# Kernel tuning notes

Hardware: AMD Instinct MI355X
Metric: run time of the kernel (lower is better)

The kernel has to match this reference:

```python
import math
import jax, jax.numpy as jnp
import numpy as np

B, T, C = 4, 2048, 2048
LAYER_ID, N_LAYER = 12, 24


def setup_inputs() -> dict:
    key = jax.random.key(0)
    kx, kk, kv, kr, ko = jax.random.split(key, 5)
    x = jax.random.normal(kx, (B, T, C), dtype=jnp.float32)

    # parameter init faithful to the torch __init__
    ratio_1_to_almost0 = 1.0 - LAYER_ID / N_LAYER
    ratio_0_to_1 = LAYER_ID / (N_LAYER - 1)
    h = np.arange(C, dtype=np.float64)
    zigzag = (((np.arange(C) + 1) % 3) - 1) * 0.5
    time_first = jnp.asarray(np.ones(C) * math.log(0.3) + zigzag, dtype=jnp.float32)
    base = (h / C)  # x[0,0,i] = i / n_embed
    time_mix_k = jnp.asarray((base ** ratio_1_to_almost0)[None, None, :], dtype=jnp.float32)
    time_mix_v = jnp.asarray((base ** ratio_1_to_almost0 + 0.3 * ratio_0_to_1)[None, None, :], dtype=jnp.float32)
    time_mix_r = jnp.asarray((base ** (0.5 * ratio_1_to_almost0))[None, None, :], dtype=jnp.float32)
    xx = jnp.ones((1, 1, C), dtype=jnp.float32)
    aa = jnp.ones((1, 1, C), dtype=jnp.float32)
    bb = jnp.ones((1, 1, C), dtype=jnp.float32)
    pp = jnp.full((1, 1, C), -1e30, dtype=jnp.float32)

    scale = 0.02
    w_key = jax.random.normal(kk, (C, C), dtype=jnp.float32) * scale
    w_value = jax.random.normal(kv, (C, C), dtype=jnp.float32) * scale
    w_rec = jax.random.normal(kr, (C, C), dtype=jnp.float32) * scale
    w_out = jax.random.normal(ko, (C, C), dtype=jnp.float32) * scale

    return {"x": x, "time_first": time_first, "time_mix_k": time_mix_k,
            "time_mix_v": time_mix_v, "time_mix_r": time_mix_r,
            "xx": xx, "aa": aa, "bb": bb, "pp": pp,
            "w_key": w_key, "w_value": w_value, "w_rec": w_rec, "w_out": w_out}


def reference(x, time_first, time_mix_k, time_mix_v, time_mix_r,
              xx, aa, bb, pp, w_key, w_value, w_rec, w_out):
    # token-mix against the (constant) xx state, broadcast over (B,T)
    xk = x * time_mix_k + (1.0 - time_mix_k) * xx
    xv = x * time_mix_v + (1.0 - time_mix_v) * xx
    xr = x * time_mix_r + (1.0 - time_mix_r) * xx

    # nn.Linear(bias=False): y = x @ W^T
    k = jnp.einsum('btc,oc->bto', xk, w_key)
    v = jnp.einsum('btc,oc->bto', xv, w_value)
    r = jax.nn.sigmoid(jnp.einsum('btc,oc->bto', xr, w_rec))

    t = x.shape[1]
    # F.pad(state, (0,0, 0,t-1, 0,0)) -> (1, T, C), zeros for t > 0
    aa_p = jnp.pad(aa, ((0, 0), (0, t - 1), (0, 0)))
    bb_p = jnp.pad(bb, ((0, 0), (0, t - 1), (0, 0)))
    pp_p = jnp.pad(pp, ((0, 0), (0, t - 1), (0, 0)))

    ww = time_first + k                      # (B,T,C)
    qq = jnp.maximum(pp_p, ww)
    e1 = jnp.exp(pp_p - qq)
    e2 = jnp.exp(ww - qq)
    wkv = (e1 * aa_p + e2 * v) / (e1 * bb_p + e2)

    return jnp.einsum('btc,oc->bto', r * wkv, w_out)
```

## Files before the change

kernel.cpp:

```cpp
#include <hip/hip_runtime.h>
#include <hip/hip_bf16.h>
#include <cstdint>
#include <cstddef>

using bf16    = __bf16;
using bf16x8  = __attribute__((ext_vector_type(8))) __bf16;
using floatx4 = __attribute__((ext_vector_type(4))) float;


__device__ __forceinline__ void async_cp16(const bf16* g, bf16* l) {
    __builtin_amdgcn_global_load_lds(
        (__attribute__((address_space(1))) void*)const_cast<bf16*>(g),
        (__attribute__((address_space(3))) void*)l,
        16, 0, 0);
}

template <int VM>
__device__ __forceinline__ void wait_vm() {
    if constexpr (VM == 8)      asm volatile("s_waitcnt vmcnt(8)" ::: "memory");
    else if constexpr (VM == 4) asm volatile("s_waitcnt vmcnt(4)" ::: "memory");
    else if constexpr (VM == 0) asm volatile("s_waitcnt vmcnt(0)" ::: "memory");
}

__device__ __forceinline__ void barrier_pin() {
    __builtin_amdgcn_s_barrier();
    __builtin_amdgcn_sched_barrier(0);
}

__global__ __launch_bounds__(256) void prep3(
    const float* __restrict__ x, const float* __restrict__ tmv,
    const float* __restrict__ tmr, const float* __restrict__ xxp,
    const float* __restrict__ wv, const float* __restrict__ wr,
    const float* __restrict__ wo, bf16* __restrict__ xb,
    bf16* __restrict__ wvb, bf16* __restrict__ wrb, bf16* __restrict__ wob,
    float* __restrict__ pV, float* __restrict__ pR,
    int C, int prepRows) {
    __shared__ float red[4][16];
    const int t  = threadIdx.x;
    const int p  = t >> 6, l = t & 63;
    const int c0 = blockIdx.x << 7;
    const int k  = c0 + (p << 5) + ((l >> 4) << 3);
    const int yb = blockIdx.y;
    const int C4 = C >> 4;

    if (yb < prepRows) {
        const int row = (yb << 4) + (l & 15);
        const float4* xi = (const float4*)&x[(size_t)row * C + k];
        const float4 a0 = xi[0], a1 = xi[1];
        const float xa[8] = {a0.x, a0.y, a0.z, a0.w, a1.x, a1.y, a1.z, a1.w};
        bf16x8 ov;
#pragma unroll
        for (int u = 0; u < 8; ++u) ov[u] = (bf16)xa[u];
        const size_t off = ((size_t)yb * (C >> 5) + (c0 >> 5) + p) * 512 + l * 8;
        *(bf16x8*)&xb[off] = ov;
    } else {
        int z = yb - prepRows;
        const float* wsrc; bf16* wdst; const float* sv = nullptr;
        float* bdst = nullptr; int mix = 1;
        if (z < C4)          { wsrc = wv; wdst = wvb; sv = tmv; bdst = pV; }
        else if (z < 2 * C4) { wsrc = wr; wdst = wrb; sv = tmr; bdst = pR; z -= C4; }
        else                 { wsrc = wo; wdst = wob; mix = 0; z -= 2 * C4; }
        const int row = (z << 4) + (l & 15);
        const float4* wi = (const float4*)&wsrc[(size_t)row * C + k];
        const float4 b0 = wi[0], b1 = wi[1];
        const float wa[8] = {b0.x, b0.y, b0.z, b0.w, b1.x, b1.y, b1.z, b1.w};
        bf16x8 ov;
        if (mix) {
            const float4 s0 = *(const float4*)&sv[k],  s1 = *(const float4*)&sv[k + 4];
            const float4 q0 = *(const float4*)&xxp[k], q1 = *(const float4*)&xxp[k + 4];
            const float sa[8] = {s0.x, s0.y, s0.z, s0.w, s1.x, s1.y, s1.z, s1.w};
            const float qa[8] = {q0.x, q0.y, q0.z, q0.w, q1.x, q1.y, q1.z, q1.w};
            float part = 0.f;
#pragma unroll
            for (int u = 0; u < 8; ++u) {
                part += (1.0f - sa[u]) * qa[u] * wa[u];
                ov[u] = (bf16)(wa[u] * sa[u]);
            }
            part += __shfl_xor(part, 16);
            part += __shfl_xor(part, 32);
            if (l < 16) red[p][l] = part;
            __syncthreads();
            if (t < 16) {
                const float s = red[0][t] + red[1][t] + red[2][t] + red[3][t];
                bdst[(size_t)(c0 >> 7) * C + (z << 4) + t] = s;
            }
        } else {
#pragma unroll
            for (int u = 0; u < 8; ++u) ov[u] = (bf16)wa[u];
        }
        const size_t off = ((size_t)z * (C >> 5) + (c0 >> 5) + p) * 512 + l * 8;
        *(bf16x8*)&wdst[off] = ov;
    }
}

__global__ __launch_bounds__(512, 2) void gemm_vr4(
    const bf16* __restrict__ XB, const bf16* __restrict__ WVB,
    const bf16* __restrict__ WRB, const float* __restrict__ pV,
    const float* __restrict__ pR, bf16* __restrict__ RW,
    int M, int N, int K) {
    __shared__ __align__(16) bf16 lds[65536];

    const int bid    = blockIdx.x;
    const int xcd    = bid & 7;
    const int tt     = bid >> 3;
    const int mtPerX = (M >> 8) >> 3;
    const int mt     = xcd * mtPerX + (tt % mtPerX);
    const int nt     = tt / mtPerX;
    const int m0     = mt << 8;
    const int n0     = nt << 7;

    const int tid  = threadIdx.x;
    const int wave = tid >> 6;
    const int lane = tid & 63;
    const int quad = lane >> 4;
    const int l16  = lane & 15;
    const int wm   = (wave >> 2) << 7;
    const int wn   = (wave & 3) << 5;
    const int xrb  = (wave >> 2) << 3;
    const int wjb  = (wave & 3) << 1;
    const int KS   = K >> 5;
    const int Q    = K >> 5;

    const bf16* gsrc;
    int grb, ldsOff;
    if (wave < 4)      { gsrc = XB;  grb = (m0 >> 4) + wave * 4;       ldsOff = wave * 2048; }
    else if (wave < 6) { gsrc = WVB; grb = (n0 >> 4) + (wave - 4) * 4; ldsOff = 8192 + (wave - 4) * 2048; }
    else               { gsrc = WRB; grb = (n0 >> 4) + (wave - 6) * 4; ldsOff = 12288 + (wave - 6) * 2048; }
    const size_t rstep = (size_t)KS * 512;
    const bf16* g0 = gsrc + (size_t)grb * rstep + lane * 8;

    floatx4 accv[8][2], accr[8][2];
#pragma unroll
    for (int i = 0; i < 8; ++i)
#pragma unroll
        for (int j = 0; j < 2; ++j) {
            accv[i][j] = (floatx4){0.f, 0.f, 0.f, 0.f};
            accr[i][j] = (floatx4){0.f, 0.f, 0.f, 0.f};
        }

    for (int s = 0; s < 3; ++s) {
        bf16* dst = &lds[s * 16384 + ldsOff];
        async_cp16(g0,             dst);
        async_cp16(g0 + rstep,     dst + 512);
        async_cp16(g0 + 2 * rstep, dst + 1024);
        async_cp16(g0 + 3 * rstep, dst + 1536);
        g0 += 512;
    }
    wait_vm<8>();
    barrier_pin();

#define VR_SLICE(q, DO_STAGE, VMEND)                                           \
    {                                                                          \
        const bf16* sb = &lds[((q) & 3) * 16384];                              \
        if (DO_STAGE) {                                                        \
            bf16* dst = &lds[(((q) + 3) & 3) * 16384 + ldsOff];                \
            async_cp16(g0,             dst);                                   \
            async_cp16(g0 + rstep,     dst + 512);                             \
            async_cp16(g0 + 2 * rstep, dst + 1024);                            \
            async_cp16(g0 + 3 * rstep, dst + 1536);                            \
            g0 += 512;                                                         \
        }                                                                      \
        bf16x8 xf[8], wvf[2], wrf[2];                                          \
        _Pragma("unroll")                                                      \
        for (int i = 0; i < 8; ++i)                                            \
            xf[i] = *(const bf16x8*)&sb[(xrb + i) * 512 + (lane << 3)];        \
        _Pragma("unroll")                                                      \
        for (int j = 0; j < 2; ++j) {                                          \
            wvf[j] = *(const bf16x8*)&sb[8192 + (wjb + j) * 512 + (lane << 3)];\
            wrf[j] = *(const bf16x8*)&sb[12288 + (wjb + j) * 512 + (lane << 3)];\
        }                                                                      \
        __builtin_amdgcn_s_setprio(1);                                         \
        _Pragma("unroll")                                                      \
        for (int i = 0; i < 8; ++i)                                            \
            _Pragma("unroll")                                                  \
            for (int j = 0; j < 2; ++j) {                                      \
                accv[i][j] = __builtin_amdgcn_mfma_f32_16x16x32_bf16(          \
                    xf[i], wvf[j], accv[i][j], 0, 0, 0);                       \
                accr[i][j] = __builtin_amdgcn_mfma_f32_16x16x32_bf16(          \
                    xf[i], wrf[j], accr[i][j], 0, 0, 0);                       \
            }                                                                  \
        __builtin_amdgcn_s_setprio(0);                                         \
        wait_vm<VMEND>();                                                      \
        barrier_pin();                                                         \
    }

    for (int q = 0; q < Q - 3; ++q) VR_SLICE(q, 1, 8)
    VR_SLICE(Q - 3, 0, 4)
    VR_SLICE(Q - 2, 0, 0)
    VR_SLICE(Q - 1, 0, -1)
#undef VR_SLICE

#pragma unroll
    for (int j = 0; j < 2; ++j) {
        const int col = n0 + wn + j * 16 + l16;
        float bvj = 0.f, brj = 0.f;
#pragma unroll
        for (int s = 0; s < 16; ++s) {
            bvj += pV[(size_t)s * N + col];
            brj += pR[(size_t)s * N + col];
        }
        const size_t cbase = (size_t)(col >> 5) * 512 +
                             (size_t)(((col >> 3) & 3) << 4) * 8 + (col & 7);
#pragma unroll
        for (int i = 0; i < 8; ++i) {
            const int rbg = ((m0 + wm) >> 4) + i;
            const size_t base = (size_t)rbg * (N >> 5) * 512 + cbase;
#pragma unroll
            for (int r = 0; r < 4; ++r) {
                const float vv = accv[i][j][r] + bvj;
                const float rr = accr[i][j][r] + brj;
                const float sg = 1.0f / (1.0f + __expf(-rr));
                RW[base + (size_t)(quad * 4 + r) * 8] = (bf16)(sg * vv);
            }
        }
    }
}

__global__ __launch_bounds__(512, 2) void gemm_o4(
    const bf16* __restrict__ AB, const bf16* __restrict__ WB,
    float* __restrict__ Of, int M, int N, int K) {
    __shared__ __align__(16) bf16 lds[65536];

    const int bid    = blockIdx.x;
    const int xcd    = bid & 7;
    const int tt     = bid >> 3;
    const int mtPerX = (M >> 8) >> 3;
    const int mt     = xcd * mtPerX + (tt % mtPerX);
    const int nt     = tt / mtPerX;
    const int m0     = mt << 8;
    const int n0     = nt << 8;

    const int tid  = threadIdx.x;
    const int wave = tid >> 6;
    const int lane = tid & 63;
    const int quad = lane >> 4;
    const int l16  = lane & 15;
    const int wm   = (wave >> 2) << 7;
    const int wn   = (wave & 3) << 6;
    const int xrb  = (wave >> 2) << 3;
    const int wjb  = (wave & 3) << 2;
    const int KS   = K >> 5;
    const int Q    = K >> 5;

    const bf16* gsrc;
    int grb, ldsOff;
    if (wave < 4) { gsrc = AB; grb = (m0 >> 4) + wave * 4;       ldsOff = wave * 2048; }
    else          { gsrc = WB; grb = (n0 >> 4) + (wave - 4) * 4; ldsOff = 8192 + (wave - 4) * 2048; }
    const size_t rstep = (size_t)KS * 512;
    const bf16* g0 = gsrc + (size_t)grb * rstep + lane * 8;

    floatx4 acc[8][4];
#pragma unroll
    for (int i = 0; i < 8; ++i)
#pragma unroll
        for (int j = 0; j < 4; ++j) acc[i][j] = (floatx4){0.f, 0.f, 0.f, 0.f};

    for (int s = 0; s < 3; ++s) {
        bf16* dst = &lds[s * 16384 + ldsOff];
        async_cp16(g0,             dst);
        async_cp16(g0 + rstep,     dst + 512);
        async_cp16(g0 + 2 * rstep, dst + 1024);
        async_cp16(g0 + 3 * rstep, dst + 1536);
        g0 += 512;
    }
    wait_vm<8>();
    barrier_pin();

#define O_SLICE(q, DO_STAGE, VMEND)                                            \
    {                                                                          \
        const bf16* sb = &lds[((q) & 3) * 16384];                              \
        if (DO_STAGE) {                                                        \
            bf16* dst = &lds[(((q) + 3) & 3) * 16384 + ldsOff];                \
            async_cp16(g0,             dst);                                   \
            async_cp16(g0 + rstep,     dst + 512);                             \
            async_cp16(g0 + 2 * rstep, dst + 1024);                            \
            async_cp16(g0 + 3 * rstep, dst + 1536);                            \
            g0 += 512;                                                         \
        }                                                                      \
        bf16x8 xf[8], wf[4];                                                   \
        _Pragma("unroll")                                                      \
        for (int i = 0; i < 8; ++i)                                            \
            xf[i] = *(const bf16x8*)&sb[(xrb + i) * 512 + (lane << 3)];        \
        _Pragma("unroll")                                                      \
        for (int j = 0; j < 4; ++j)                                            \
            wf[j] = *(const bf16x8*)&sb[8192 + (wjb + j) * 512 + (lane << 3)]; \
        __builtin_amdgcn_s_setprio(1);                                         \
        _Pragma("unroll")                                                      \
        for (int i = 0; i < 8; ++i)                                            \
            _Pragma("unroll")                                                  \
            for (int j = 0; j < 4; ++j)                                        \
                acc[i][j] = __builtin_amdgcn_mfma_f32_16x16x32_bf16(           \
                    xf[i], wf[j], acc[i][j], 0, 0, 0);                         \
        __builtin_amdgcn_s_setprio(0);                                         \
        wait_vm<VMEND>();                                                      \
        barrier_pin();                                                         \
    }

    for (int q = 0; q < Q - 3; ++q) O_SLICE(q, 1, 8)
    O_SLICE(Q - 3, 0, 4)
    O_SLICE(Q - 2, 0, 0)
    O_SLICE(Q - 1, 0, -1)
#undef O_SLICE

#pragma unroll
    for (int i = 0; i < 8; ++i) {
        const int row0 = m0 + wm + i * 16 + quad * 4;
#pragma unroll
        for (int j = 0; j < 4; ++j) {
            const int col = n0 + wn + j * 16 + l16;
#pragma unroll
            for (int r = 0; r < 4; ++r)
                Of[(size_t)(row0 + r) * N + col] = acc[i][j][r];
        }
    }
}

extern "C" void kernel_launch(void* const* d_in, const int* in_sizes, int n_in,
                              void* d_out, int out_size, void* d_ws, size_t ws_size,
                              hipStream_t stream) {
    const int C = in_sizes[1];
    const int M = in_sizes[0] / C;
    const size_t MC = (size_t)M * C;
    const size_t CC = (size_t)C * C;

    const float* x   = (const float*)d_in[0];
    const float* tmv = (const float*)d_in[3];
    const float* tmr = (const float*)d_in[4];
    const float* xxp = (const float*)d_in[5];
    const float* wv  = (const float*)d_in[10];
    const float* wr  = (const float*)d_in[11];
    const float* wo  = (const float*)d_in[12];

    uint8_t* ws = (uint8_t*)d_ws;
    bf16* xb    = (bf16*)ws;
    bf16* rwkv  = (bf16*)(ws + MC * 2);
    bf16* wvb   = (bf16*)(ws + MC * 4);
    bf16* wrb   = (bf16*)(ws + MC * 4 + CC * 2);
    bf16* wob   = (bf16*)(ws + MC * 4 + CC * 4);
    float* pV   = (float*)(ws + MC * 4 + CC * 6);
    float* pR   = pV + 16 * (size_t)C;
    const size_t need = MC * 4 + CC * 6 + (size_t)C * 128;
    if (ws_size < need) return;

    dim3 gridP(C / 128, M / 16 + 3 * (C / 16));
    prep3<<<gridP, 256, 0, stream>>>(x, tmv, tmr, xxp, wv, wr, wo,
                                     xb, wvb, wrb, wob, pV, pR, C, M / 16);
    gemm_vr4<<<(M / 256) * (C / 128), 512, 0, stream>>>(xb, wvb, wrb, pV, pR,
                                                        rwkv, M, C, C);
    gemm_o4<<<(M / 256) * (C / 256), 512, 0, stream>>>(rwkv, wob, (float*)d_out,
                                                       M, C, C);
}
```

Baseline: 353.1 us.

## Double-buffer A fragments in registers, prefetching next slice before MFMAs

Both GEMM kernels now load the next K-slice's X/A fragments from LDS into a second register set while the current slice's MFMAs run, ping-ponging between two fragment arrays. The global-to-LDS wait schedule is tightened (vmcnt 4 instead of 8) so the next stage is resident one iteration earlier. The goal is to hide LDS read latency behind matrix math. In exchange it raises VGPR pressure with 512-thread, 2-block launch bounds, which may cause spills or lower occupancy, and it waits earlier on global loads.

After: 350.7 us. No clear change (-0.7%).

```diff
diff --git a/kernel.cpp b/kernel.cpp
--- a/kernel.cpp
+++ b/kernel.cpp
@@ -17,8 +17,7 @@
 
 template <int VM>
 __device__ __forceinline__ void wait_vm() {
-    if constexpr (VM == 8)      asm volatile("s_waitcnt vmcnt(8)" ::: "memory");
-    else if constexpr (VM == 4) asm volatile("s_waitcnt vmcnt(4)" ::: "memory");
+    if constexpr (VM == 4) asm volatile("s_waitcnt vmcnt(4)" ::: "memory");
     else if constexpr (VM == 0) asm volatile("s_waitcnt vmcnt(0)" ::: "memory");
 }
 
@@ -93,7 +92,7 @@
     }
 }
 
-__global__ __launch_bounds__(512, 2) void gemm_vr4(
+__global__ __launch_bounds__(512, 2) void gemm_vr5(
     const bf16* __restrict__ XB, const bf16* __restrict__ WVB,
     const bf16* __restrict__ WRB, const float* __restrict__ pV,
     const float* __restrict__ pR, bf16* __restrict__ RW,
@@ -146,12 +145,18 @@
         async_cp16(g0 + 3 * rstep, dst + 1536);
         g0 += 512;
     }
-    wait_vm<8>();
+    wait_vm<4>();
     barrier_pin();
 
-#define VR_SLICE(q, DO_STAGE, VMEND)                                           \
+    bf16x8 xfA[8], xfB[8];
+#pragma unroll
+    for (int i = 0; i < 8; ++i)
+        xfA[i] = *(const bf16x8*)&lds[(xrb + i) * 512 + (lane << 3)];
+
+#define VR_SLICE(q, XIN, XOUT, DO_STAGE, VMODE, DO_PF)                         \
     {                                                                          \
-        const bf16* sb = &lds[((q) & 3) * 16384];                              \
+        const bf16* sb  = &lds[((q) & 3) * 16384];                             \
+        const bf16* sbn = &lds[(((q) + 1) & 3) * 16384];                       \
         if (DO_STAGE) {                                                        \
             bf16* dst = &lds[(((q) + 3) & 3) * 16384 + ldsOff];                \
             async_cp16(g0,             dst);                                   \
@@ -160,34 +165,41 @@
             async_cp16(g0 + 3 * rstep, dst + 1536);                            \
             g0 += 512;                                                         \
         }                                                                      \
-        bf16x8 xf[8], wvf[2], wrf[2];                                          \
-        _Pragma("unroll")                                                      \
-        for (int i = 0; i < 8; ++i)                                            \
-            xf[i] = *(const bf16x8*)&sb[(xrb + i) * 512 + (lane << 3)];        \
+        bf16x8 wvf[2], wrf[2];                                                 \
         _Pragma("unroll")                                                      \
         for (int j = 0; j < 2; ++j) {                                          \
             wvf[j] = *(const bf16x8*)&sb[8192 + (wjb + j) * 512 + (lane << 3)];\
             wrf[j] = *(const bf16x8*)&sb[12288 + (wjb + j) * 512 + (lane << 3)];\
         }                                                                      \
+        if (DO_PF) {                                                           \
+            _Pragma("unroll")                                                  \
+            for (int i = 0; i < 8; ++i)                                        \
+                XOUT[i] = *(const bf16x8*)&sbn[(xrb + i) * 512 + (lane << 3)]; \
+        }                                                                      \
         __builtin_amdgcn_s_setprio(1);                                         \
         _Pragma("unroll")                                                      \
-        for (int i = 0; i < 8; ++i)                                            \
-            _Pragma("unroll")                                                  \
-            for (int j = 0; j < 2; ++j) {                                      \
-                accv[i][j] = __builtin_amdgcn_mfma_f32_16x16x32_bf16(          \
-                    xf[i], wvf[j], accv[i][j], 0, 0, 0);                       \
-                accr[i][j] = __builtin_amdgcn_mfma_f32_16x16x32_bf16(          \
-                    xf[i], wrf[j], accr[i][j], 0, 0, 0);                       \
-            }                                                                  \
+        for (int i = 0; i < 8; ++i) {                                          \
+            accv[i][0] = __builtin_amdgcn_mfma_f32_16x16x32_bf16(              \
+                XIN[i], wvf[0], accv[i][0], 0, 0, 0);                          \
+            accv[i][1] = __builtin_amdgcn_mfma_f32_16x16x32_bf16(              \
+                XIN[i], wvf[1], accv[i][1], 0, 0, 0);                          \
+            accr[i][0] = __builtin_amdgcn_mfma_f32_16x16x32_bf16(              \
+                XIN[i], wrf[0], accr[i][0], 0, 0, 0);                          \
+            accr[i][1] = __builtin_amdgcn_mfma_f32_16x16x32_bf16(              \
+                XIN[i], wrf[1], accr[i][1], 0, 0, 0);                          \
+        }                                                                      \
         __builtin_amdgcn_s_setprio(0);                                         \
-        wait_vm<VMEND>();                                                      \
+        if ((VMODE) == 0) wait_vm<4>();                                        \
+        else if ((VMODE) == 1) wait_vm<0>();                                   \
         barrier_pin();                                                         \
     }
 
-    for (int q = 0; q < Q - 3; ++q) VR_SLICE(q, 1, 8)
-    VR_SLICE(Q - 3, 0, 4)
-    VR_SLICE(Q - 2, 0, 0)
-    VR_SLICE(Q - 1, 0, -1)
+    for (int q = 0; q < Q - 2; q += 2) {
+        VR_SLICE(q,     xfA, xfB, (q     <= Q - 4), ((q     <= Q - 4) ? 0 : 1), 1)
+        VR_SLICE(q + 1, xfB, xfA, (q + 1 <= Q - 4), ((q + 1 <= Q - 4) ? 0 : 1), 1)
+    }
+    VR_SLICE(Q - 2, xfA, xfB, 0, 2, 1)
+    VR_SLICE(Q - 1, xfB, xfA, 0, 2, 0)
 #undef VR_SLICE
 
 #pragma unroll
@@ -216,7 +228,7 @@
     }
 }
 
-__global__ __launch_bounds__(512, 2) void gemm_o4(
+__global__ __launch_bounds__(512, 2) void gemm_o5(
     const bf16* __restrict__ AB, const bf16* __restrict__ WB,
     float* __restrict__ Of, int M, int N, int K) {
     __shared__ __align__(16) bf16 lds[65536];
@@ -263,12 +275,18 @@
         async_cp16(g0 + 3 * rstep, dst + 1536);
         g0 += 512;
     }
-    wait_vm<8>();
+    wait_vm<4>();
     barrier_pin();
 
-#define O_SLICE(q, DO_STAGE, VMEND)                                            \
+    bf16x8 xfA[8], xfB[8];
+#pragma unroll
+    for (int i = 0; i < 8; ++i)
+        xfA[i] = *(const bf16x8*)&lds[(xrb + i) * 512 + (lane << 3)];
+
+#define O_SLICE(q, XIN, XOUT, DO_STAGE, VMODE, DO_PF)                          \
     {                                                                          \
-        const bf16* sb = &lds[((q) & 3) * 16384];                              \
+        const bf16* sb  = &lds[((q) & 3) * 16384];                             \
+        const bf16* sbn = &lds[(((q) + 1) & 3) * 16384];                       \
         if (DO_STAGE) {                                                        \
             bf16* dst = &lds[(((q) + 3) & 3) * 16384 + ldsOff];                \
             async_cp16(g0,             dst);                                   \
@@ -277,29 +295,34 @@
             async_cp16(g0 + 3 * rstep, dst + 1536);                            \
             g0 += 512;                                                         \
         }                                                                      \
-        bf16x8 xf[8], wf[4];                                                   \
-        _Pragma("unroll")                                                      \
-        for (int i = 0; i < 8; ++i)                                            \
-            xf[i] = *(const bf16x8*)&sb[(xrb + i) * 512 + (lane << 3)];        \
+        bf16x8 wf[4];                                                          \
         _Pragma("unroll")                                                      \
         for (int j = 0; j < 4; ++j)                                            \
             wf[j] = *(const bf16x8*)&sb[8192 + (wjb + j) * 512 + (lane << 3)]; \
+        if (DO_PF) {                                                           \
+            _Pragma("unroll")                                                  \
+            for (int i = 0; i < 8; ++i)                                        \
+                XOUT[i] = *(const bf16x8*)&sbn[(xrb + i) * 512 + (lane << 3)]; \
+        }                                                                      \
         __builtin_amdgcn_s_setprio(1);                                         \
         _Pragma("unroll")                                                      \
         for (int i = 0; i < 8; ++i)                                            \
             _Pragma("unroll")                                                  \
             for (int j = 0; j < 4; ++j)                                        \
                 acc[i][j] = __builtin_amdgcn_mfma_f32_16x16x32_bf16(           \
-                    xf[i], wf[j], acc[i][j], 0, 0, 0);                         \
+                    XIN[i], wf[j], acc[i][j], 0, 0, 0);                        \
         __builtin_amdgcn_s_setprio(0);                                         \
-        wait_vm<VMEND>();                                                      \
+        if ((VMODE) == 0) wait_vm<4>();                                        \
+        else if ((VMODE) == 1) wait_vm<0>();                                   \
         barrier_pin();                                                         \
     }
 
-    for (int q = 0; q < Q - 3; ++q) O_SLICE(q, 1, 8)
-    O_SLICE(Q - 3, 0, 4)
-    O_SLICE(Q - 2, 0, 0)
-    O_SLICE(Q - 1, 0, -1)
+    for (int q = 0; q < Q - 2; q += 2) {
+        O_SLICE(q,     xfA, xfB, (q     <= Q - 4), ((q     <= Q - 4) ? 0 : 1), 1)
+        O_SLICE(q + 1, xfB, xfA, (q + 1 <= Q - 4), ((q + 1 <= Q - 4) ? 0 : 1), 1)
+    }
+    O_SLICE(Q - 2, xfA, xfB, 0, 2, 1)
+    O_SLICE(Q - 1, xfB, xfA, 0, 2, 0)
 #undef O_SLICE
 
 #pragma unroll
@@ -345,8 +368,8 @@
     dim3 gridP(C / 128, M / 16 + 3 * (C / 16));
     prep3<<<gridP, 256, 0, stream>>>(x, tmv, tmr, xxp, wv, wr, wo,
                                      xb, wvb, wrb, wob, pV, pR, C, M / 16);
-    gemm_vr4<<<(M / 256) * (C / 128), 512, 0, stream>>>(xb, wvb, wrb, pV, pR,
+    gemm_vr5<<<(M / 256) * (C / 128), 512, 0, stream>>>(xb, wvb, wrb, pV, pR,
                                                         rwkv, M, C, C);
-    gemm_o4<<<(M / 256) * (C / 256), 512, 0, stream>>>(rwkv, wob, (float*)d_out,
+    gemm_o5<<<(M / 256) * (C / 256), 512, 0, stream>>>(rwkv, wob, (float*)d_out,
                                                        M, C, C);
 }
```
